# Kernel optimization log

Measured on AMD Instinct MI355X. Metric: run time of the kernel, lower is better.

The kernel has to match this reference:

```python
import jax, jax.numpy as jnp
import numpy as np

B, C, NMAX = 16, 1, 256
H = 128          # hidden_dim == embedding_dim
KATT = 64        # att_edge_dim
L = 2            # num_GNN_layers
NPROP = 1        # num_GNN_prop
M = 400000       # num edges
EPRED = 400000   # num predicted node pairs
NNODE = 20000    # num GNN nodes
KMIX = 20        # num_mix_component
EIN = H + 2 * KATT


def setup_inputs() -> dict:
    key = jax.random.key(0)
    ks = iter(jax.random.split(key, 40))
    def nrm(shape, s=0.05):
        return jax.random.normal(next(ks), shape, jnp.float32) * s
    inp = {}
    inp["A_pad"] = jax.random.normal(next(ks), (B, C, NMAX, NMAX), jnp.float32)
    inp["edges"] = jax.random.randint(next(ks), (M, 2), 0, NNODE)
    inp["node_idx_gnn"] = jax.random.randint(next(ks), (EPRED, 2), 0, NNODE)
    inp["node_idx_feat"] = jax.random.randint(next(ks), (NNODE,), 0, B * C * NMAX + 1)
    inp["att_idx"] = jax.random.randint(next(ks), (NNODE,), 0, 2)
    inp["W_in"] = nrm((NMAX, H)); inp["b_in"] = jnp.zeros(H)
    inp["msg_W1"] = nrm((L, EIN, H)); inp["msg_b1"] = jnp.zeros((L, H))
    inp["msg_W2"] = nrm((L, H, H)); inp["msg_b2"] = jnp.zeros((L, H))
    inp["att_W1"] = nrm((L, EIN, H)); inp["att_b1"] = jnp.zeros((L, H))
    inp["att_W2"] = nrm((L, H, H)); inp["att_b2"] = jnp.zeros((L, H))
    inp["gru_Wih"] = nrm((L, H, 3 * H)); inp["gru_bih"] = jnp.zeros((L, 3 * H))
    inp["gru_Whh"] = nrm((L, H, 3 * H)); inp["gru_bhh"] = jnp.zeros((L, 3 * H))
    inp["theta_W1"] = nrm((H, H)); inp["theta_b1"] = jnp.zeros(H)
    inp["theta_W2"] = nrm((H, H)); inp["theta_b2"] = jnp.zeros(H)
    inp["theta_W3"] = nrm((H, KMIX)); inp["theta_b3"] = jnp.zeros(KMIX)
    inp["alpha_W1"] = nrm((H, H)); inp["alpha_b1"] = jnp.zeros(H)
    inp["alpha_W2"] = nrm((H, H)); inp["alpha_b2"] = jnp.zeros(H)
    inp["alpha_W3"] = nrm((H, KMIX)); inp["alpha_b3"] = jnp.zeros(KMIX)
    return inp


def _gru(x, h, Wih, bih, Whh, bhh):
    # torch GRUCell gate order: r, z, n
    gi = x @ Wih + bih
    gh = h @ Whh + bhh
    ir, iz, in_ = jnp.split(gi, 3, axis=1)
    hr, hz, hn = jnp.split(gh, 3, axis=1)
    r = jax.nn.sigmoid(ir + hr)
    z = jax.nn.sigmoid(iz + hz)
    n = jnp.tanh(in_ + r * hn)
    return (1.0 - z) * n + z * h


def _forward(A_pad, W_in, b_in, msg_W1, msg_b1, msg_W2, msg_b2,
             att_W1, att_b1, att_W2, att_b2,
             gru_Wih, gru_bih, gru_Whh, gru_bhh,
             theta_W1, theta_b1, theta_W2, theta_b2, theta_W3, theta_b3,
             alpha_W1, alpha_b1, alpha_W2, alpha_b2, alpha_W3, alpha_b3,
             edges, node_idx_gnn, node_idx_feat, att_idx):
    nmax = A_pad.shape[-1]
    # decoder_input + zero pad row at front
    node_feat = A_pad.reshape(-1, nmax) @ W_in + b_in              # [B*C*Nmax, H]
    node_feat = jnp.pad(node_feat, ((1, 0), (0, 0)))
    src, dst = edges[:, 0], edges[:, 1]
    m = edges.shape[0]
    rows = jnp.arange(m)
    aef = jnp.zeros((m, 2 * KATT), A_pad.dtype)                    # one-hot att edge feat
    aef = aef.at[rows, att_idx[src]].set(1.0)
    aef = aef.at[rows, att_idx[dst] + KATT].set(1.0)
    state = node_feat[node_idx_feat]                               # [N_node, H]
    n_node = node_idx_feat.shape[0]
    for l in range(L):
        if l > 0:
            state = jax.nn.relu(state)
        for _ in range(NPROP):
            diff = state[src] - state[dst]                         # edge gather
            ei = jnp.concatenate([diff, aef], axis=1)              # [M, H+2*KATT]
            msg = jax.nn.relu(ei @ msg_W1[l] + msg_b1[l]) @ msg_W2[l] + msg_b2[l]
            att = jax.nn.sigmoid(jax.nn.relu(ei @ att_W1[l] + att_b1[l]) @ att_W2[l] + att_b2[l])
            agg = jax.ops.segment_sum(msg * att, dst, num_segments=n_node)
            state = _gru(agg, state, gru_Wih[l], gru_bih[l], gru_Whh[l], gru_bhh[l])
    d = state[node_idx_gnn[:, 0]] - state[node_idx_gnn[:, 1]]      # [E_pred, H]
    h1 = jax.nn.relu(d @ theta_W1 + theta_b1)
    h1 = jax.nn.relu(h1 @ theta_W2 + theta_b2)
    log_theta = h1 @ theta_W3 + theta_b3                           # [E_pred, KMIX]
    h2 = jax.nn.relu(d @ alpha_W1 + alpha_b1)
    h2 = jax.nn.relu(h2 @ alpha_W2 + alpha_b2)
    log_alpha = jax.nn.log_softmax(h2 @ alpha_W3 + alpha_b3, axis=1)
    return log_theta, log_alpha


def reference(A_pad, edges, node_idx_gnn, node_idx_feat, att_idx,
              W_in, b_in, msg_W1, msg_b1, msg_W2, msg_b2,
              att_W1, att_b1, att_W2, att_b2,
              gru_Wih, gru_bih, gru_Whh, gru_bhh,
              theta_W1, theta_b1, theta_W2, theta_b2, theta_W3, theta_b3,
              alpha_W1, alpha_b1, alpha_W2, alpha_b2, alpha_W3, alpha_b3):
    return _forward(A_pad, W_in, b_in, msg_W1, msg_b1, msg_W2, msg_b2,
                    att_W1, att_b1, att_W2, att_b2,
                    gru_Wih, gru_bih, gru_Whh, gru_bhh,
                    theta_W1, theta_b1, theta_W2, theta_b2, theta_W3, theta_b3,
                    alpha_W1, alpha_b1, alpha_W2, alpha_b2, alpha_W3, alpha_b3,
                    edges, node_idx_gnn, node_idx_feat, att_idx)
```

## Files before the change

kernel.cpp:

```cpp
#include <hip/hip_runtime.h>
#include <hip/hip_bf16.h>

#define H 128
#define KMIX 20

using f32x4 = __attribute__((ext_vector_type(4))) float;
using bf8v  = __attribute__((ext_vector_type(8))) short;
using fv4   = __attribute__((ext_vector_type(4))) float;
using iv4   = __attribute__((ext_vector_type(4))) int;

#define OFF_MW1T 0
#define OFF_MW2T 32768
#define OFF_AW1T 65536
#define OFF_AW2T 98304
#define OFF_WIHT 131072
#define OFF_WHHT 229376
#define OFF_TW1T 327680
#define OFF_TW2T 344064
#define OFF_TW3T 360448
#define OFF_PW1T 364544
#define OFF_PW2T 380928
#define OFF_PW3T 397312
#define OFF_WINT 401408
#define WTOTAL   434176

__device__ __forceinline__ short f2bf(float x){
  union { __hip_bfloat16 h; unsigned short u; } cv;
  cv.h = __float2bfloat16(x);
  return (short)cv.u;
}
__device__ __forceinline__ float bf2f(short b){
  union { unsigned u; float f; } v; v.u = ((unsigned)(unsigned short)b) << 16;
  return v.f;
}
__device__ __forceinline__ f32x4 mfma16(bf8v a, bf8v b, f32x4 c){
  return __builtin_amdgcn_mfma_f32_16x16x32_bf16(a, b, c, 0, 0, 0);
}
__device__ __forceinline__ bf8v pack_row(const float* __restrict__ p, int ko){
  float4 s0 = *(const float4*)(p + ko);
  float4 s1 = *(const float4*)(p + ko + 4);
  bf8v t;
  t[0]=f2bf(s0.x); t[1]=f2bf(s0.y); t[2]=f2bf(s0.z); t[3]=f2bf(s0.w);
  t[4]=f2bf(s1.x); t[5]=f2bf(s1.y); t[6]=f2bf(s1.z); t[7]=f2bf(s1.w);
  return t;
}
__device__ __forceinline__ bf8v pack_row_nt(const float* __restrict__ p, int ko){
  fv4 s0 = __builtin_nontemporal_load((const fv4*)(p + ko));
  fv4 s1 = __builtin_nontemporal_load((const fv4*)(p + ko + 4));
  bf8v t;
  t[0]=f2bf(s0[0]); t[1]=f2bf(s0[1]); t[2]=f2bf(s0[2]); t[3]=f2bf(s0[3]);
  t[4]=f2bf(s1[0]); t[5]=f2bf(s1[1]); t[6]=f2bf(s1[2]); t[7]=f2bf(s1[3]);
  return t;
}
__device__ __forceinline__ bf8v relu_db(bf8v s, bf8v d, const float* __restrict__ bias){
  float4 c0 = *(const float4*)(bias);
  float4 c1 = *(const float4*)(bias + 4);
  float cv[8] = {c0.x,c0.y,c0.z,c0.w,c1.x,c1.y,c1.z,c1.w};
  bf8v t;
#pragma unroll
  for (int j=0;j<8;j++){
    float v = bf2f(s[j]) - bf2f(d[j]) + cv[j];
    t[j] = f2bf(v > 0.f ? v : 0.f);
  }
  return t;
}

__global__ void prep_kernel(
    const float* __restrict__ msg_W1, const float* __restrict__ msg_W2,
    const float* __restrict__ att_W1, const float* __restrict__ att_W2,
    const float* __restrict__ gru_Wih, const float* __restrict__ gru_Whh,
    const float* __restrict__ theta_W1, const float* __restrict__ theta_W2, const float* __restrict__ theta_W3,
    const float* __restrict__ alpha_W1, const float* __restrict__ alpha_W2, const float* __restrict__ alpha_W3,
    const float* __restrict__ W_in, const float* __restrict__ msg_b1, const float* __restrict__ att_b1,
    short* __restrict__ wb, float* __restrict__ cbm, float* __restrict__ cba)
{
  const int j = blockIdx.x, tid = threadIdx.x;
  if (j < 12){
    const float* src; short* dst;
    switch(j){
      case 0:  src = msg_W1;             dst = wb + OFF_MW1T;        break;
      case 1:  src = msg_W1 + 256*128;   dst = wb + OFF_MW1T+16384;  break;
      case 2:  src = msg_W2;             dst = wb + OFF_MW2T;        break;
      case 3:  src = msg_W2 + 128*128;   dst = wb + OFF_MW2T+16384;  break;
      case 4:  src = att_W1;             dst = wb + OFF_AW1T;        break;
      case 5:  src = att_W1 + 256*128;   dst = wb + OFF_AW1T+16384;  break;
      case 6:  src = att_W2;             dst = wb + OFF_AW2T;        break;
      case 7:  src = att_W2 + 128*128;   dst = wb + OFF_AW2T+16384;  break;
      case 8:  src = theta_W1;           dst = wb + OFF_TW1T;        break;
      case 9:  src = theta_W2;           dst = wb + OFF_TW2T;        break;
      case 10: src = alpha_W1;           dst = wb + OFF_PW1T;        break;
      default: src = alpha_W2;           dst = wb + OFF_PW2T;        break;
    }
    for (int i = tid; i < 128*128; i += 256){
      int q = (i>>9)&31, kk = q&3, nt = q>>2;
      int lane = (i>>3)&63, jj = i&7;
      int n = nt*16 + (lane&15), k = kk*32 + (lane>>4)*8 + jj;
      dst[i] = f2bf(src[k*128 + n]);
    }
  } else if (j < 16){
    int q = j - 12;
    const float* src = (q < 2 ? gru_Wih : gru_Whh) + (q & 1) * 128*384;
    short* dst = wb + (q < 2 ? OFF_WIHT : OFF_WHHT) + (q & 1) * 49152;
    for (int i = tid; i < 3*128*128; i += 256){
      int g = i >> 14, rem = i & 16383;
      int qq = (rem>>9)&31, kk = qq&3, nt = qq>>2;
      int lane = (rem>>3)&63, jj = rem&7;
      int n = nt*16 + (lane&15), k = kk*32 + (lane>>4)*8 + jj;
      dst[i] = f2bf(src[k*384 + g*128 + n]);
    }
  } else if (j < 18){
    const float* src = (j == 16) ? theta_W3 : alpha_W3;
    short* dst = wb + ((j == 16) ? OFF_TW3T : OFF_PW3T);
    for (int i = tid; i < 32*128; i += 256){
      int q = i>>9, kk = q&3, nt = q>>2;
      int lane = (i>>3)&63, jj = i&7;
      int n = nt*16 + (lane&15), k = kk*32 + (lane>>4)*8 + jj;
      dst[i] = (n < KMIX) ? f2bf(src[k*KMIX + n]) : (short)0;
    }
  } else if (j == 18){
    for (int i = tid; i < 128*256; i += 256){
      int q = i>>9, kk = q&7, nt = q>>3;
      int lane = (i>>3)&63, jj = i&7;
      int n = nt*16 + (lane&15), k = kk*32 + (lane>>4)*8 + jj;
      wb[OFF_WINT + i] = f2bf(W_in[k*128 + n]);
    }
  } else {
    for (int i = tid; i < 2048; i += 256){
      int path = i >> 10, rem = i & 1023;
      int l = rem >> 9, rem2 = rem & 511;
      int combo = rem2 >> 7, c = rem2 & 127;
      int a = combo >> 1, b = combo & 1;
      const float* W  = path ? att_W1 : msg_W1;
      const float* bb = path ? att_b1 : msg_b1;
      float v = bb[l*128 + c] + W[(l*256 + 128 + a)*128 + c] + W[(l*256 + 192 + b)*128 + c];
      float* dst = path ? cba : cbm;
      dst[(l*4 + combo)*128 + c] = v;
    }
  }
}

__global__ void hist_kernel(const int* __restrict__ edges, int* __restrict__ counts, int M){
  int i = blockIdx.x*256 + threadIdx.x;
  if (i < M) atomicAdd(&counts[edges[2*i+1]], 1);
}

__global__ __launch_bounds__(1024)
void scanA_kernel(const int* __restrict__ counts, int* __restrict__ offs,
                  int* __restrict__ btot, int NK)
{
  __shared__ int buf[1024];
  const int tid = threadIdx.x;
  int i = blockIdx.x*1024 + tid;
  int v = (i < NK) ? counts[i] : 0;
  buf[tid] = v; __syncthreads();
#pragma unroll
  for (int off = 1; off < 1024; off <<= 1){
    int t = (tid >= off) ? buf[tid-off] : 0;
    __syncthreads();
    buf[tid] += t;
    __syncthreads();
  }
  if (i < NK) offs[i] = buf[tid] - v;
  if (tid == 1023) btot[blockIdx.x] = buf[1023];
}

__global__ __launch_bounds__(1024)
void scanB_kernel(int* __restrict__ btot, int NBLK)
{
  __shared__ int buf[1024];
  const int tid = threadIdx.x;
  int v = (tid < NBLK) ? btot[tid] : 0;
  buf[tid] = v; __syncthreads();
#pragma unroll
  for (int off = 1; off < 1024; off <<= 1){
    int t = (tid >= off) ? buf[tid-off] : 0;
    __syncthreads();
    buf[tid] += t;
    __syncthreads();
  }
  if (tid < NBLK) btot[tid] = buf[tid] - v;
}

__global__ __launch_bounds__(1024)
void scanC_kernel(int* __restrict__ offs, const int* __restrict__ btot,
                  int* __restrict__ cursor, int NK, int M)
{
  int i = blockIdx.x*1024 + threadIdx.x;
  if (i < NK){
    int o = offs[i] + btot[blockIdx.x];
    offs[i] = o;
    cursor[i] = o;
  }
  if (i == 0) offs[NK] = M;
}

__global__ void scatter_kernel(const int* __restrict__ edges, const int* __restrict__ att_idx,
                               int* __restrict__ cursor, int* __restrict__ spk,
                               int* __restrict__ sdst, int M)
{
  int i = blockIdx.x*256 + threadIdx.x;
  if (i >= M) return;
  int s = edges[2*i], d = edges[2*i+1];
  int p = atomicAdd(&cursor[d], 1);
  spk[p] = s | ((att_idx[s]*2 + att_idx[d]) << 20);
  sdst[p] = d;
}

__global__ __launch_bounds__(256)
void nodefeat_kernel(const float* __restrict__ A, const short* __restrict__ WinT,
                     const float* __restrict__ b_in, float* __restrict__ nf)
{
  const int tid = threadIdx.x, wave = tid>>6, lane = tid&63;
  const int col = lane&15, khi = lane>>4;
  const int rbase = blockIdx.x*64 + wave*16;
  const float* pa = A + (size_t)(rbase + col)*256;
  bf8v a[8];
#pragma unroll
  for (int kk=0;kk<8;kk++) a[kk] = pack_row_nt(pa, kk*32 + khi*8);
#pragma unroll
  for (int nt=0;nt<8;nt++){
    float bv = b_in[nt*16+col];
    f32x4 c = {bv,bv,bv,bv};
#pragma unroll
    for (int kk=0;kk<8;kk++){
      bf8v b = *(const bf8v*)(WinT + ((nt*8+kk)<<9) + (lane<<3));
      c = mfma16(a[kk], b, c);
    }
#pragma unroll
    for (int r=0;r<4;r++)
      nf[(size_t)(rbase + khi*4 + r)*H + nt*16+col] = c[r];
  }
}

__global__ void gather_kernel(const float* __restrict__ nf, const int* __restrict__ nif,
                              float* __restrict__ st, int NN)
{
  int i = blockIdx.x*256 + threadIdx.x;
  if (i >= NN*32) return;
  int v = i >> 5, c = i & 31;
  int idx = nif[v];
  float4 val = {0.f,0.f,0.f,0.f};
  if (idx > 0) val = *(const float4*)(nf + (size_t)(idx-1)*H + c*4);
  *(float4*)(st + (size_t)v*H + c*4) = val;
}

__global__ __launch_bounds__(256)
void nodemm_kernel(const float* __restrict__ x,
                   const short* __restrict__ WT1, const short* __restrict__ WT2,
                   short* __restrict__ o1, short* __restrict__ o2, int ostr, int NN)
{
  const int tid = threadIdx.x, wave = tid>>6, lane = tid&63;
  const int col = lane&15, khi = lane>>4;
  const int nbase = blockIdx.x*64 + wave*16;
  if (nbase >= NN) return;
  const float* px = x + (size_t)(nbase + col)*H;
  bf8v a[4];
#pragma unroll
  for (int kk=0;kk<4;kk++) a[kk] = pack_row(px, kk*32 + khi*8);
#pragma unroll
  for (int m=0;m<2;m++){
    const short* Wt = m ? WT2 : WT1;
    short* o = m ? o2 : o1;
#pragma unroll
    for (int nt=0;nt<8;nt++){
      f32x4 c = {0.f,0.f,0.f,0.f};
#pragma unroll
      for (int kk=0;kk<4;kk++){
        bf8v b = *(const bf8v*)(Wt + ((nt*4+kk)<<9) + (lane<<3));
        c = mfma16(a[kk], b, c);
      }
#pragma unroll
      for (int r=0;r<4;r++)
        o[(size_t)(nbase + khi*4 + r)*ostr + nt*16+col] = f2bf(c[r]);
    }
  }
}

__global__ __launch_bounds__(256,3)
void edge_kernel(const short* __restrict__ UV,
                 const int* __restrict__ spk, const int* __restrict__ sdst,
                 const short* __restrict__ mW2T, const short* __restrict__ aW2T,
                 const float* __restrict__ cbm, const float* __restrict__ cba,
                 const float* __restrict__ mb2, const float* __restrict__ ab2,
                 short* __restrict__ msgbuf, int M)
{
  __shared__ __align__(16) char smem[4][8192];
  const int tid = threadIdx.x, wave = tid>>6, lane = tid&63;
  const int col = lane&15, khi = lane>>4;
  const int pbase = blockIdx.x*128 + wave*32;
  if (pbase >= M) return;
  char* lds = smem[wave];

  bf8v usr[2][4], vsr[2][4];
  int dA[2], cmA[2];
#pragma unroll
  for (int t=0;t<2;t++){
    const int p = pbase + t*16 + col;
    const int v = spk[p];
    dA[t] = sdst[p];
    cmA[t] = v >> 20;
    const short* us = UV + (size_t)(v & 0xFFFFF)*256;
#pragma unroll
    for (int kk=0;kk<4;kk++){
      int ko = kk*32 + khi*8;
      usr[t][kk] = *(const bf8v*)(us+ko);
      vsr[t][kk] = *(const bf8v*)(us+128+ko);
    }
  }
  bf8v am[2][4], aa[2][4];
#pragma unroll
  for (int t=0;t<2;t++){
    const short* ud = UV + (size_t)dA[t]*256;
    const float* cbmp = cbm + cmA[t]*H;
    const float* cbap = cba + cmA[t]*H;
#pragma unroll
    for (int kk=0;kk<4;kk++){
      int ko = kk*32 + khi*8;
      am[t][kk] = relu_db(usr[t][kk], *(const bf8v*)(ud+ko),     cbmp+ko);
      aa[t][kk] = relu_db(vsr[t][kk], *(const bf8v*)(ud+128+ko), cbap+ko);
    }
  }
#pragma unroll
  for (int nt=0;nt<8;nt++){
    f32x4 c[2], c2[2];
#pragma unroll
    for (int t=0;t<2;t++){ c[t] = (f32x4){0.f,0.f,0.f,0.f}; c2[t] = (f32x4){0.f,0.f,0.f,0.f}; }
#pragma unroll
    for (int kk=0;kk<4;kk++){
      bf8v bm = *(const bf8v*)(mW2T + ((nt*4+kk)<<9) + (lane<<3));
      bf8v ba = *(const bf8v*)(aW2T + ((nt*4+kk)<<9) + (lane<<3));
#pragma unroll
      for (int t=0;t<2;t++){
        c[t]  = mfma16(am[t][kk], bm, c[t]);
        c2[t] = mfma16(aa[t][kk], ba, c2[t]);
      }
    }
    int cc = nt*16 + col;
    float bm2 = mb2[cc], ba2 = ab2[cc];
#pragma unroll
    for (int t=0;t<2;t++){
#pragma unroll
      for (int r=0;r<4;r++){
        float m  = c[t][r] + bm2;
        float sg = 1.f/(1.f + __expf(-(c2[t][r] + ba2)));
        int row = khi*4 + r;
        int bo = (t<<12) + (row<<8) + cc*2;
        bo ^= ((khi&3)<<5) ^ ((r&1)<<4);
        *(short*)(lds + bo) = f2bf(m*sg);
      }
    }
  }
#pragma unroll
  for (int t=0;t<2;t++){
#pragma unroll
    for (int i=0;i<4;i++){
      int row = i*4 + khi;
      int bo = (t<<12) + (row<<8) + col*16;
      bo ^= (((row>>2)&3)<<5) ^ ((row&1)<<4);
      iv4 w = *(const iv4*)(lds + bo);
      __builtin_nontemporal_store(w,
          (iv4*)(msgbuf + (size_t)(pbase + t*16 + row)*H) + col);
    }
  }
}

__global__ __launch_bounds__(256)
void agg_kernel(const short* __restrict__ msgbuf, const int* __restrict__ offs,
                float* __restrict__ agg, int NN)
{
  const int tid = threadIdx.x, wave = tid>>6, lane = tid&63;
  const int v = blockIdx.x*4 + wave;
  if (v >= NN) return;
  const int p0 = offs[v], p1 = offs[v+1];
  const unsigned* base = (const unsigned*)msgbuf;
  float a0 = 0.f, a1 = 0.f, b0 = 0.f, b1 = 0.f;
  int p = p0;
  for (; p + 4 <= p1; p += 4){
    unsigned m0 = __builtin_nontemporal_load(base + (size_t)p*64 + lane);
    unsigned m1 = __builtin_nontemporal_load(base + (size_t)(p+1)*64 + lane);
    unsigned m2 = __builtin_nontemporal_load(base + (size_t)(p+2)*64 + lane);
    unsigned m3 = __builtin_nontemporal_load(base + (size_t)(p+3)*64 + lane);
    a0 += bf2f((short)(m0 & 0xffff)) + bf2f((short)(m2 & 0xffff));
    a1 += bf2f((short)(m0 >> 16))    + bf2f((short)(m2 >> 16));
    b0 += bf2f((short)(m1 & 0xffff)) + bf2f((short)(m3 & 0xffff));
    b1 += bf2f((short)(m1 >> 16))    + bf2f((short)(m3 >> 16));
  }
  for (; p < p1; ++p){
    unsigned m0 = __builtin_nontemporal_load(base + (size_t)p*64 + lane);
    a0 += bf2f((short)(m0 & 0xffff));
    a1 += bf2f((short)(m0 >> 16));
  }
  float2 o; o.x = a0 + b0; o.y = a1 + b1;
  *(float2*)(agg + (size_t)v*H + lane*2) = o;
}

__global__ __launch_bounds__(256)
void gru_uv_kernel(const float* __restrict__ xa, const float* __restrict__ hs,
                   const short* __restrict__ WihT, const short* __restrict__ WhhT,
                   const float* __restrict__ bih, const float* __restrict__ bhh,
                   float* __restrict__ stOut,
                   const short* __restrict__ W1a, const short* __restrict__ W1b,
                   short* __restrict__ o1, short* __restrict__ o2, int ostr,
                   int NN, int relu_out)
{
  __shared__ float smem[4][16][132];
  const int tid = threadIdx.x, wave = tid>>6, lane = tid&63;
  const int col = lane&15, khi = lane>>4;
  const int nbase = blockIdx.x*64 + wave*16;
  if (nbase >= NN) return;
  float (*tile)[132] = smem[wave];

  const float* px = xa + (size_t)(nbase + col)*H;
  const float* ph = hs + (size_t)(nbase + col)*H;
  bf8v ax[4], ah[4];
#pragma unroll
  for (int kk=0;kk<4;kk++){
    ax[kk] = pack_row(px, kk*32 + khi*8);
    ah[kk] = pack_row(ph, kk*32 + khi*8);
  }
#pragma unroll
  for (int nt=0;nt<8;nt++){
    f32x4 ar = {0.f,0.f,0.f,0.f}, az = {0.f,0.f,0.f,0.f};
    f32x4 ani = {0.f,0.f,0.f,0.f}, anh = {0.f,0.f,0.f,0.f};
    int nc = nt*16 + col;
#pragma unroll
    for (int kk=0;kk<4;kk++){
      int fo = ((nt*4+kk)<<9) + (lane<<3);
      ar  = mfma16(ax[kk], *(const bf8v*)(WihT + fo), ar);
      ar  = mfma16(ah[kk], *(const bf8v*)(WhhT + fo), ar);
      az  = mfma16(ax[kk], *(const bf8v*)(WihT + 16384 + fo), az);
      az  = mfma16(ah[kk], *(const bf8v*)(WhhT + 16384 + fo), az);
      ani = mfma16(ax[kk], *(const bf8v*)(WihT + 32768 + fo), ani);
      anh = mfma16(ah[kk], *(const bf8v*)(WhhT + 32768 + fo), anh);
    }
    float br  = bih[nc] + bhh[nc];
    float bz  = bih[128+nc] + bhh[128+nc];
    float bni = bih[256+nc], bnh = bhh[256+nc];
#pragma unroll
    for (int r=0;r<4;r++){
      int row = nbase + khi*4 + r;
      float rr = 1.f/(1.f + __expf(-(ar[r] + br)));
      float zz = 1.f/(1.f + __expf(-(az[r] + bz)));
      float nn = tanhf(ani[r] + bni + rr*(anh[r] + bnh));
      float h  = hs[(size_t)row*H + nc];
      float o  = (1.f - zz)*nn + zz*h;
      if (relu_out) o = o > 0.f ? o : 0.f;
      if (stOut) stOut[(size_t)row*H + nc] = o;
      tile[khi*4 + r][nc] = o;
    }
  }
  bf8v a[4];
#pragma unroll
  for (int kk=0;kk<4;kk++) a[kk] = pack_row(&tile[col][0], kk*32 + khi*8);
#pragma unroll
  for (int m=0;m<2;m++){
    const short* Wt = m ? W1b : W1a;
    short* o = m ? o2 : o1;
#pragma unroll
    for (int nt=0;nt<8;nt++){
      f32x4 c = {0.f,0.f,0.f,0.f};
#pragma unroll
      for (int kk=0;kk<4;kk++){
        bf8v b = *(const bf8v*)(Wt + ((nt*4+kk)<<9) + (lane<<3));
        c = mfma16(a[kk], b, c);
      }
#pragma unroll
      for (int r=0;r<4;r++)
        o[(size_t)(nbase + khi*4 + r)*ostr + nt*16+col] = f2bf(c[r]);
    }
  }
}

__global__ __launch_bounds__(256,3)
void pred_kernel(const short* __restrict__ Pt, const short* __restrict__ Pa,
                 const int* __restrict__ nig,
                 const short* __restrict__ tW2T, const short* __restrict__ tW3T,
                 const float* __restrict__ tb1, const float* __restrict__ tb2, const float* __restrict__ tb3,
                 const short* __restrict__ pW2T, const short* __restrict__ pW3T,
                 const float* __restrict__ pb1, const float* __restrict__ pb2, const float* __restrict__ pb3,
                 float* __restrict__ outT, float* __restrict__ outA, int E)
{
  __shared__ __align__(16) unsigned char smem[4][8192];
  __shared__ __align__(16) float osmem[4][640];
  const int path = blockIdx.y;
  const short* P   = path ? Pa   : Pt;
  const short* W2T = path ? pW2T : tW2T;
  const short* W3T = path ? pW3T : tW3T;
  const float* b1  = path ? pb1  : tb1;
  const float* b2  = path ? pb2  : tb2;
  const float* b3  = path ? pb3  : tb3;
  float* out       = path ? outA : outT;
  const int tid = threadIdx.x, wave = tid>>6, lane = tid&63;
  const int col = lane&15, khi = lane>>4;
  const int ebase = blockIdx.x*128 + wave*32;
  if (ebase >= E) return;
  unsigned char* lds = &smem[wave][0];
  float* ost = osmem[wave];

  bf8v p0r[2][4], p1r[2][4];
#pragma unroll
  for (int t=0;t<2;t++){
    int e = ebase + t*16 + col;
    const short* q0 = P + (size_t)nig[2*e]*H;
    const short* q1 = P + (size_t)nig[2*e+1]*H;
#pragma unroll
    for (int kk=0;kk<4;kk++){
      int ko = kk*32 + khi*8;
      p0r[t][kk] = *(const bf8v*)(q0+ko);
      p1r[t][kk] = *(const bf8v*)(q1+ko);
    }
  }
  bf8v a1[2][4];
#pragma unroll
  for (int t=0;t<2;t++)
#pragma unroll
    for (int kk=0;kk<4;kk++){
      int ko = kk*32 + khi*8;
      a1[t][kk] = relu_db(p0r[t][kk], p1r[t][kk], b1+ko);
    }
#pragma unroll
  for (int nt=0;nt<8;nt++){
    float bv = b2[nt*16+col];
    f32x4 c[2];
#pragma unroll
    for (int t=0;t<2;t++) c[t] = (f32x4){bv,bv,bv,bv};
#pragma unroll
    for (int kk=0;kk<4;kk++){
      bf8v b = *(const bf8v*)(W2T + ((nt*4+kk)<<9) + (lane<<3));
#pragma unroll
      for (int t=0;t<2;t++) c[t] = mfma16(a1[t][kk], b, c[t]);
    }
#pragma unroll
    for (int t=0;t<2;t++)
#pragma unroll
      for (int r=0;r<4;r++){
        int row = t*16 + khi*4 + r, cc = nt*16 + col;
        float v = c[t][r]; v = v > 0.f ? v : 0.f;
        *(unsigned short*)(lds + ((row*256 + cc*2) ^ ((row&7)<<4))) = (unsigned short)f2bf(v);
      }
  }
#pragma unroll
  for (int t=0;t<2;t++){
    bf8v a3[4];
#pragma unroll
    for (int kk=0;kk<4;kk++){
      int row = t*16 + col;
      int cb = kk*64 + khi*16;
      a3[kk] = *(const bf8v*)(lds + ((row*256 + cb) ^ ((row&7)<<4)));
    }
    f32x4 c3[2];
#pragma unroll
    for (int nt=0;nt<2;nt++){
      f32x4 c = {0.f,0.f,0.f,0.f};
#pragma unroll
      for (int kk=0;kk<4;kk++){
        bf8v b = *(const bf8v*)(W3T + ((nt*4+kk)<<9) + (lane<<3));
        c = mfma16(a3[kk], b, c);
      }
      c3[nt] = c;
    }
    if (!path){
#pragma unroll
      for (int r=0;r<4;r++){
        int el = t*16 + khi*4 + r;
        ost[el*KMIX + col] = c3[0][r] + b3[col];
        if (col < 4) ost[el*KMIX + 16 + col] = c3[1][r] + b3[16+col];
      }
    } else {
#pragma unroll
      for (int r=0;r<4;r++){
        float v0 = c3[0][r] + b3[col];
        float v1 = (col < 4) ? (c3[1][r] + b3[16+col]) : -1e30f;
        float mx = fmaxf(v0, v1);
#pragma unroll
        for (int mk=1; mk<16; mk<<=1) mx = fmaxf(mx, __shfl_xor(mx, mk, 64));
        float se = __expf(v0-mx) + ((col < 4) ? __expf(v1-mx) : 0.f);
#pragma unroll
        for (int mk=1; mk<16; mk<<=1) se += __shfl_xor(se, mk, 64);
        float lse = mx + __logf(se);
        int el = t*16 + khi*4 + r;
        ost[el*KMIX + col] = v0 - lse;
        if (col < 4) ost[el*KMIX + 16 + col] = v1 - lse;
      }
    }
  }
  {
    fv4* dst = (fv4*)(out + (size_t)ebase*KMIX);
    const fv4* src = (const fv4*)ost;
#pragma unroll
    for (int i=0;i<2;i++)
      __builtin_nontemporal_store(src[lane + i*64], dst + lane + i*64);
    if (lane < 32)
      __builtin_nontemporal_store(src[lane + 128], dst + lane + 128);
  }
}

extern "C" void kernel_launch(void* const* d_in, const int* in_sizes, int n_in,
                              void* d_out, int out_size, void* d_ws, size_t ws_size,
                              hipStream_t stream)
{
  (void)n_in; (void)out_size; (void)ws_size;
  const float* A_pad   = (const float*)d_in[0];
  const int*   edges   = (const int*)d_in[1];
  const int*   nig     = (const int*)d_in[2];
  const int*   nif     = (const int*)d_in[3];
  const int*   atti    = (const int*)d_in[4];
  const float* W_in    = (const float*)d_in[5];
  const float* b_in    = (const float*)d_in[6];
  const float* msg_W1  = (const float*)d_in[7];
  const float* msg_b1  = (const float*)d_in[8];
  const float* msg_W2  = (const float*)d_in[9];
  const float* msg_b2  = (const float*)d_in[10];
  const float* att_W1  = (const float*)d_in[11];
  const float* att_b1  = (const float*)d_in[12];
  const float* att_W2  = (const float*)d_in[13];
  const float* att_b2  = (const float*)d_in[14];
  const float* gru_Wih = (const float*)d_in[15];
  const float* gru_bih = (const float*)d_in[16];
  const float* gru_Whh = (const float*)d_in[17];
  const float* gru_bhh = (const float*)d_in[18];
  const float* theta_W1 = (const float*)d_in[19];
  const float* theta_b1 = (const float*)d_in[20];
  const float* theta_W2 = (const float*)d_in[21];
  const float* theta_b2 = (const float*)d_in[22];
  const float* theta_W3 = (const float*)d_in[23];
  const float* theta_b3 = (const float*)d_in[24];
  const float* alpha_W1 = (const float*)d_in[25];
  const float* alpha_b1 = (const float*)d_in[26];
  const float* alpha_W2 = (const float*)d_in[27];
  const float* alpha_b2 = (const float*)d_in[28];
  const float* alpha_W3 = (const float*)d_in[29];
  const float* alpha_b3 = (const float*)d_in[30];

  const int M  = in_sizes[1] / 2;
  const int EP = in_sizes[2] / 2;
  const int NN = in_sizes[3];

  char* p = (char*)d_ws;
  float* node_feat = (float*)p; p += (size_t)4096*H*4;
  float* stateA    = (float*)p; p += (size_t)NN*H*4;
  float* stateB    = (float*)p; p += (size_t)NN*H*4;
  float* agg       = (float*)p; p += (size_t)NN*H*4;
  short* UV        = (short*)p; p += (size_t)NN*256*2;
  short* U         = (short*)p; p += (size_t)NN*H*2;
  short* Vv        = (short*)p; p += (size_t)NN*H*2;
  short* wb        = (short*)p; p += (size_t)WTOTAL*2;
  float* cbm       = (float*)p; p += 2*4*H*4;
  float* cba       = (float*)p; p += 2*4*H*4;
  int*   counts    = (int*)p;  p += (size_t)(NN+4)*4;
  int*   offs      = (int*)p;  p += (size_t)(NN+4)*4;
  int*   cursor    = (int*)p;  p += (size_t)(NN+4)*4;
  int*   btot      = (int*)p;  p += (size_t)1024*4;
  int*   spk       = (int*)p;  p += (size_t)M*4;
  int*   sdst      = (int*)p;  p += (size_t)M*4;
  short* msgbuf    = (short*)p; p += (size_t)M*H*2;

  float* outT = (float*)d_out;
  float* outA = outT + (size_t)EP*KMIX;

  prep_kernel<<<20,256,0,stream>>>(msg_W1,msg_W2,att_W1,att_W2,gru_Wih,gru_Whh,
      theta_W1,theta_W2,theta_W3,alpha_W1,alpha_W2,alpha_W3,W_in,msg_b1,att_b1,
      wb,cbm,cba);
  nodefeat_kernel<<<64,256,0,stream>>>(A_pad, wb+OFF_WINT, b_in, node_feat);
  gather_kernel<<<(NN*32+255)/256,256,0,stream>>>(node_feat, nif, stateA, NN);

  const int NBLK = (NN + 1023) / 1024;
  (void)hipMemsetAsync(counts, 0, (size_t)NN*4, stream);
  hist_kernel<<<(M+255)/256,256,0,stream>>>(edges, counts, M);
  scanA_kernel<<<NBLK,1024,0,stream>>>(counts, offs, btot, NN);
  scanB_kernel<<<1,1024,0,stream>>>(btot, NBLK);
  scanC_kernel<<<NBLK,1024,0,stream>>>(offs, btot, cursor, NN, M);
  scatter_kernel<<<(M+255)/256,256,0,stream>>>(edges, atti, cursor, spk, sdst, M);

  nodemm_kernel<<<(NN+63)/64,256,0,stream>>>(stateA,
      wb+OFF_MW1T, wb+OFF_AW1T, UV, UV+128, 256, NN);

  edge_kernel<<<(M+127)/128,256,0,stream>>>(UV, spk, sdst,
      wb+OFF_MW2T, wb+OFF_AW2T, cbm, cba, msg_b2, att_b2, msgbuf, M);
  agg_kernel<<<(NN+3)/4,256,0,stream>>>(msgbuf, offs, agg, NN);
  gru_uv_kernel<<<(NN+63)/64,256,0,stream>>>(agg, stateA,
      wb+OFF_WIHT, wb+OFF_WHHT, gru_bih, gru_bhh, stateB,
      wb+OFF_MW1T+16384, wb+OFF_AW1T+16384, UV, UV+128, 256, NN, 1);

  edge_kernel<<<(M+127)/128,256,0,stream>>>(UV, spk, sdst,
      wb+OFF_MW2T+16384, wb+OFF_AW2T+16384, cbm+4*H, cba+4*H,
      msg_b2+H, att_b2+H, msgbuf, M);
  agg_kernel<<<(NN+3)/4,256,0,stream>>>(msgbuf, offs, agg, NN);
  gru_uv_kernel<<<(NN+63)/64,256,0,stream>>>(agg, stateB,
      wb+OFF_WIHT+49152, wb+OFF_WHHT+49152, gru_bih+384, gru_bhh+384, (float*)nullptr,
      wb+OFF_TW1T, wb+OFF_PW1T, U, Vv, 128, NN, 0);

  pred_kernel<<<dim3((EP+127)/128,2),256,0,stream>>>(U, Vv, nig,
      wb+OFF_TW2T, wb+OFF_TW3T, theta_b1, theta_b2, theta_b3,
      wb+OFF_PW2T, wb+OFF_PW3T, alpha_b1, alpha_b2, alpha_b3,
      outT, outA, EP);
}
```

Measured before the change: 553.7 us.

## Fuse message aggregation into edge kernel via segmented atomics; fuse gather into nodemm

The edge kernel no longer writes per-edge bf16 messages to a global buffer that a separate agg kernel re-reads. Instead each wave reduces its 32 destination-sorted edges in LDS and emits float atomicAdds to agg once per run of equal destinations, with agg zeroed by a memset beforehand. Separately, the initial state gather is folded into the first node matmul kernel, which writes stateA while packing its inputs. This removes roughly 100MB of message traffic per layer and two launches, at the cost of float atomics, which make summation order nondeterministic, and extra memsets.

```diff
diff --git a/kernel.cpp b/kernel.cpp
--- a/kernel.cpp
+++ b/kernel.cpp
@@ -232,31 +232,33 @@
   }
 }
 
-__global__ void gather_kernel(const float* __restrict__ nf, const int* __restrict__ nif,
-                              float* __restrict__ st, int NN)
-{
-  int i = blockIdx.x*256 + threadIdx.x;
-  if (i >= NN*32) return;
-  int v = i >> 5, c = i & 31;
-  int idx = nif[v];
-  float4 val = {0.f,0.f,0.f,0.f};
-  if (idx > 0) val = *(const float4*)(nf + (size_t)(idx-1)*H + c*4);
-  *(float4*)(st + (size_t)v*H + c*4) = val;
-}
-
 __global__ __launch_bounds__(256)
-void nodemm_kernel(const float* __restrict__ x,
-                   const short* __restrict__ WT1, const short* __restrict__ WT2,
-                   short* __restrict__ o1, short* __restrict__ o2, int ostr, int NN)
+void gnodemm_kernel(const float* __restrict__ nf, const int* __restrict__ nif,
+                    const short* __restrict__ WT1, const short* __restrict__ WT2,
+                    float* __restrict__ stOut, short* __restrict__ o1, short* __restrict__ o2,
+                    int ostr, int NN)
 {
   const int tid = threadIdx.x, wave = tid>>6, lane = tid&63;
   const int col = lane&15, khi = lane>>4;
   const int nbase = blockIdx.x*64 + wave*16;
   if (nbase >= NN) return;
-  const float* px = x + (size_t)(nbase + col)*H;
+  const int node = nbase + col;
+  const int idx = (node < NN) ? nif[node] : 0;
+  const float* px = nf + (size_t)(idx-1)*H;
   bf8v a[4];
-#pragma unroll
-  for (int kk=0;kk<4;kk++) a[kk] = pack_row(px, kk*32 + khi*8);
+  float* so = stOut + (size_t)node*H;
+#pragma unroll
+  for (int kk=0;kk<4;kk++){
+    int ko = kk*32 + khi*8;
+    float4 s0 = {0,0,0,0}, s1 = {0,0,0,0};
+    if (idx > 0){ s0 = *(const float4*)(px + ko); s1 = *(const float4*)(px + ko + 4); }
+    *(float4*)(so + ko)     = s0;
+    *(float4*)(so + ko + 4) = s1;
+    bf8v t;
+    t[0]=f2bf(s0.x); t[1]=f2bf(s0.y); t[2]=f2bf(s0.z); t[3]=f2bf(s0.w);
+    t[4]=f2bf(s1.x); t[5]=f2bf(s1.y); t[6]=f2bf(s1.z); t[7]=f2bf(s1.w);
+    a[kk] = t;
+  }
 #pragma unroll
   for (int m=0;m<2;m++){
     const short* Wt = m ? WT2 : WT1;
@@ -282,7 +284,7 @@
                  const short* __restrict__ mW2T, const short* __restrict__ aW2T,
                  const float* __restrict__ cbm, const float* __restrict__ cba,
                  const float* __restrict__ mb2, const float* __restrict__ ab2,
-                 short* __restrict__ msgbuf, int M)
+                 float* __restrict__ agg, int M)
 {
   __shared__ __align__(16) char smem[4][8192];
   const int tid = threadIdx.x, wave = tid>>6, lane = tid&63;
@@ -295,7 +297,7 @@
   int dA[2], cmA[2];
 #pragma unroll
   for (int t=0;t<2;t++){
-    const int p = pbase + t*16 + col;
+    const int p = min(pbase + t*16 + col, M-1);
     const int v = spk[p];
     dA[t] = sdst[p];
     cmA[t] = v >> 20;
@@ -350,48 +352,27 @@
       }
     }
   }
-#pragma unroll
-  for (int t=0;t<2;t++){
-#pragma unroll
-    for (int i=0;i<4;i++){
-      int row = i*4 + khi;
-      int bo = (t<<12) + (row<<8) + col*16;
-      bo ^= (((row>>2)&3)<<5) ^ ((row&1)<<4);
-      iv4 w = *(const iv4*)(lds + bo);
-      __builtin_nontemporal_store(w,
-          (iv4*)(msgbuf + (size_t)(pbase + t*16 + row)*H) + col);
-    }
-  }
-}
-
-__global__ __launch_bounds__(256)
-void agg_kernel(const short* __restrict__ msgbuf, const int* __restrict__ offs,
-                float* __restrict__ agg, int NN)
-{
-  const int tid = threadIdx.x, wave = tid>>6, lane = tid&63;
-  const int v = blockIdx.x*4 + wave;
-  if (v >= NN) return;
-  const int p0 = offs[v], p1 = offs[v+1];
-  const unsigned* base = (const unsigned*)msgbuf;
-  float a0 = 0.f, a1 = 0.f, b0 = 0.f, b1 = 0.f;
-  int p = p0;
-  for (; p + 4 <= p1; p += 4){
-    unsigned m0 = __builtin_nontemporal_load(base + (size_t)p*64 + lane);
-    unsigned m1 = __builtin_nontemporal_load(base + (size_t)(p+1)*64 + lane);
-    unsigned m2 = __builtin_nontemporal_load(base + (size_t)(p+2)*64 + lane);
-    unsigned m3 = __builtin_nontemporal_load(base + (size_t)(p+3)*64 + lane);
-    a0 += bf2f((short)(m0 & 0xffff)) + bf2f((short)(m2 & 0xffff));
-    a1 += bf2f((short)(m0 >> 16))    + bf2f((short)(m2 >> 16));
-    b0 += bf2f((short)(m1 & 0xffff)) + bf2f((short)(m3 & 0xffff));
-    b1 += bf2f((short)(m1 >> 16))    + bf2f((short)(m3 >> 16));
-  }
-  for (; p < p1; ++p){
-    unsigned m0 = __builtin_nontemporal_load(base + (size_t)p*64 + lane);
-    a0 += bf2f((short)(m0 & 0xffff));
-    a1 += bf2f((short)(m0 >> 16));
-  }
-  float2 o; o.x = a0 + b0; o.y = a1 + b1;
-  *(float2*)(agg + (size_t)v*H + lane*2) = o;
+  {
+    const int c0 = lane, c1 = lane + 64;
+    float acc0 = 0.f, acc1 = 0.f;
+    int prev = sdst[pbase];
+#pragma unroll
+    for (int g=0; g<32; ++g){
+      if (pbase + g >= M) break;
+      int dg = sdst[pbase + g];
+      if (dg != prev){
+        atomicAdd(&agg[(size_t)prev*H + c0], acc0);
+        atomicAdd(&agg[(size_t)prev*H + c1], acc1);
+        acc0 = 0.f; acc1 = 0.f; prev = dg;
+      }
+      int t = g >> 4, row = g & 15;
+      int sw = (((row>>2)&3)<<5) ^ ((row&1)<<4);
+      acc0 += bf2f(*(const short*)(lds + (((t<<12) + (row<<8) + c0*2) ^ sw)));
+      acc1 += bf2f(*(const short*)(lds + (((t<<12) + (row<<8) + c1*2) ^ sw)));
+    }
+    atomicAdd(&agg[(size_t)prev*H + c0], acc0);
+    atomicAdd(&agg[(size_t)prev*H + c1], acc1);
+  }
 }
 
 __global__ __launch_bounds__(256)
@@ -653,7 +634,6 @@
   int*   btot      = (int*)p;  p += (size_t)1024*4;
   int*   spk       = (int*)p;  p += (size_t)M*4;
   int*   sdst      = (int*)p;  p += (size_t)M*4;
-  short* msgbuf    = (short*)p; p += (size_t)M*H*2;
 
   float* outT = (float*)d_out;
   float* outA = outT + (size_t)EP*KMIX;
@@ -662,7 +642,6 @@
       theta_W1,theta_W2,theta_W3,alpha_W1,alpha_W2,alpha_W3,W_in,msg_b1,att_b1,
       wb,cbm,cba);
   nodefeat_kernel<<<64,256,0,stream>>>(A_pad, wb+OFF_WINT, b_in, node_feat);
-  gather_kernel<<<(NN*32+255)/256,256,0,stream>>>(node_feat, nif, stateA, NN);
 
   const int NBLK = (NN + 1023) / 1024;
   (void)hipMemsetAsync(counts, 0, (size_t)NN*4, stream);
@@ -672,20 +651,20 @@
   scanC_kernel<<<NBLK,1024,0,stream>>>(offs, btot, cursor, NN, M);
   scatter_kernel<<<(M+255)/256,256,0,stream>>>(edges, atti, cursor, spk, sdst, M);
 
-  nodemm_kernel<<<(NN+63)/64,256,0,stream>>>(stateA,
-      wb+OFF_MW1T, wb+OFF_AW1T, UV, UV+128, 256, NN);
-
+  gnodemm_kernel<<<(NN+63)/64,256,0,stream>>>(node_feat, nif,
+      wb+OFF_MW1T, wb+OFF_AW1T, stateA, UV, UV+128, 256, NN);
+
+  (void)hipMemsetAsync(agg, 0, (size_t)NN*H*4, stream);
   edge_kernel<<<(M+127)/128,256,0,stream>>>(UV, spk, sdst,
-      wb+OFF_MW2T, wb+OFF_AW2T, cbm, cba, msg_b2, att_b2, msgbuf, M);
-  agg_kernel<<<(NN+3)/4,256,0,stream>>>(msgbuf, offs, agg, NN);
+      wb+OFF_MW2T, wb+OFF_AW2T, cbm, cba, msg_b2, att_b2, agg, M);
   gru_uv_kernel<<<(NN+63)/64,256,0,stream>>>(agg, stateA,
       wb+OFF_WIHT, wb+OFF_WHHT, gru_bih, gru_bhh, stateB,
       wb+OFF_MW1T+16384, wb+OFF_AW1T+16384, UV, UV+128, 256, NN, 1);
 
+  (void)hipMemsetAsync(agg, 0, (size_t)NN*H*4, stream);
   edge_kernel<<<(M+127)/128,256,0,stream>>>(UV, spk, sdst,
       wb+OFF_MW2T+16384, wb+OFF_AW2T+16384, cbm+4*H, cba+4*H,
-      msg_b2+H, att_b2+H, msgbuf, M);
-  agg_kernel<<<(NN+3)/4,256,0,stream>>>(msgbuf, offs, agg, NN);
+      msg_b2+H, att_b2+H, agg, M);
   gru_uv_kernel<<<(NN+63)/64,256,0,stream>>>(agg, stateB,
       wb+OFF_WIHT+49152, wb+OFF_WHHT+49152, gru_bih+384, gru_bhh+384, (float*)nullptr,
       wb+OFF_TW1T, wb+OFF_PW1T, U, Vv, 128, NN, 0);
```

Result: no change. 548.3 us (-1.0%).
